# Kernel tuning notes

Hardware: AMD Instinct MI355X
Metric: run time of the kernel (lower is better)

Reference implementation:

```python
import jax, jax.numpy as jnp
import numpy as np

B, A, E = 16384, 8, 512


def setup_inputs() -> dict:
    key = jax.random.key(0)
    ks = jax.random.split(key, 6)
    return {
        "image_features": jax.random.normal(ks[0], (B, E), dtype=jnp.float32),
        "edge_attributes": jax.random.normal(ks[1], (B, A, E), dtype=jnp.float32),
        "linear_w": jax.random.normal(ks[2], (E, 2 * E), dtype=jnp.float32) * (1.0 / np.sqrt(2 * E)),
        "linear_b": jax.random.normal(ks[3], (E,), dtype=jnp.float32) * 0.01,
        "fwd_proj": jax.random.normal(ks[4], (A, E, E), dtype=jnp.float32) * (1.0 / np.sqrt(E)),
        "bwd_proj": jax.random.normal(ks[5], (A, E, E), dtype=jnp.float32) * (1.0 / np.sqrt(E)),
        "self_weighted": jnp.ones((1, A, 1), dtype=jnp.float32),
    }


def reference(image_features, edge_attributes, linear_w, linear_b, fwd_proj, bwd_proj, self_weighted):
    # Forward attribute GNN: broadcast src over attribute axis, concat, linear(2E->E)
    src = jnp.broadcast_to(image_features[:, None, :], edge_attributes.shape)  # [B,A,E]
    x = jnp.concatenate([src, edge_attributes], axis=-1)                       # [B,A,2E]
    agg = jnp.einsum('bak,ek->bae', x, linear_w) + linear_b                    # [B,A,E]
    attr_rep = jnp.einsum('bai,aij->baj', agg, fwd_proj)                       # [B,A,E]

    # Backward attribute GNN: per-type projection, ReLU, learned weighted sum over A
    proj = jnp.einsum('bai,aij->baj', attr_rep, bwd_proj)                      # [B,A,E]
    individuals = jnp.sum(jax.nn.relu(proj) * self_weighted, axis=1)           # [B,E]
    return attr_rep, individuals
```

## Files before the change

### kernel.cpp

```cpp
#include <hip/hip_runtime.h>
#include <cstdint>
#include <cstddef>

#define NB 16384
#define NA 8
#define NE 512
#define NK 1024
#define NN 4096

typedef __bf16 bf16x8 __attribute__((ext_vector_type(8)));
typedef float  f32x4  __attribute__((ext_vector_type(4)));
typedef uint16_t u16x8 __attribute__((ext_vector_type(8)));

__device__ __forceinline__ uint16_t cvt_bf16(float f) {
    uint32_t u = __builtin_bit_cast(uint32_t, f);
    u += 0x7fffu + ((u >> 16) & 1u);
    return (uint16_t)(u >> 16);
}

__device__ __forceinline__ int swz(int row) { return (row ^ (row >> 2)) & 3; }

__device__ __forceinline__ int cf_pos(int row, int c) {
    return ((row >> 1) << 3) + ((((row & 1) << 2) + c) ^ ((row >> 1) & 7));
}

__device__ __forceinline__ void gl_lds16(const void* g, void* l) {
    __builtin_amdgcn_global_load_lds(
        (__attribute__((address_space(1))) void*)(void*)g,
        (__attribute__((address_space(3))) void*)l, 16, 0, 0);
}

__global__ __launch_bounds__(256) void k_tcvt(const float* __restrict__ in,
                                              uint16_t* __restrict__ out,
                                              int R, int C) {
    __shared__ float tile[32][33];
    int mat = blockIdx.z;
    int c0 = blockIdx.x * 32, r0 = blockIdx.y * 32;
    int tx = threadIdx.x & 31, ty = threadIdx.x >> 5;
    const float* src = in + (size_t)mat * R * C;
    uint16_t* dst = out + (size_t)mat * R * C;
#pragma unroll
    for (int yy = 0; yy < 4; ++yy) {
        int r = ty + yy * 8;
        tile[r][tx] = src[(size_t)(r0 + r) * C + c0 + tx];
    }
    __syncthreads();
#pragma unroll
    for (int yy = 0; yy < 4; ++yy) {
        int c = ty + yy * 8;
        dst[(size_t)(c0 + c) * R + r0 + tx] = cvt_bf16(tile[tx][c]);
    }
}

__global__ __launch_bounds__(256) void k_cvt4(const float* __restrict__ in,
                                              uint16_t* __restrict__ out, int n4) {
    int i = blockIdx.x * 256 + threadIdx.x;
    if (i >= n4) return;
    float4 v = ((const float4*)in)[i];
    ushort4 o;
    o.x = cvt_bf16(v.x); o.y = cvt_bf16(v.y); o.z = cvt_bf16(v.z); o.w = cvt_bf16(v.w);
    ((ushort4*)out)[i] = o;
}

__global__ __launch_bounds__(256) void k_bvec(const float* __restrict__ lb,
                                              const float* __restrict__ fwd,
                                              float* __restrict__ bvec) {
    int a = blockIdx.x >> 4, i0 = (blockIdx.x & 15) * 32;
    int t = threadIdx.x;
    float s0 = 0.f, s1 = 0.f;
#pragma unroll 4
    for (int i = 0; i < 32; ++i) {
        float w = lb[i0 + i];
        const float* f = fwd + ((size_t)a * NE + i0 + i) * NE;
        s0 = fmaf(w, f[t], s0);
        s1 = fmaf(w, f[t + 256], s1);
    }
    atomicAdd(&bvec[a * NE + t], s0);
    atomicAdd(&bvec[a * NE + t + 256], s1);
}

__global__ __launch_bounds__(256) void k_prep(const uint16_t* __restrict__ lwT,
                                              const uint16_t* __restrict__ fwdT,
                                              uint16_t* __restrict__ TMT) {
    __shared__ alignas(16) uint16_t lA[128 * 32];
    __shared__ alignas(16) uint16_t lB[128 * 32];
    int bz = blockIdx.x;
    int nt = bz & 31, mt = bz >> 5;
    int m0 = mt * 128, n0 = nt * 128;
    int t = threadIdx.x, lane = t & 63;
    int w = t >> 6, wm = w >> 1, wn = w & 1;
    int lr = lane & 15, lc = lane >> 4;
    int sl = swz(lr);
    f32x4 acc[4][4] = {};
    for (int k0 = 0; k0 < NE; k0 += 32) {
        __syncthreads();
#pragma unroll
        for (int p = 0; p < 2; ++p) {
            int idx = p * 256 + t;
            int row = idx >> 2, c16 = (idx & 3) ^ swz(row);
            gl_lds16(lwT + (size_t)(m0 + row) * NE + k0 + c16 * 8, lA + idx * 8);
            gl_lds16(fwdT + (size_t)(n0 + row) * NE + k0 + c16 * 8, lB + idx * 8);
        }
        __syncthreads();
        bf16x8 af[4], bfr[4];
#pragma unroll
        for (int i = 0; i < 4; ++i)
            af[i] = *(const bf16x8*)&lA[(wm * 64 + i * 16 + lr) * 32 + ((lc ^ sl) << 3)];
#pragma unroll
        for (int j = 0; j < 4; ++j)
            bfr[j] = *(const bf16x8*)&lB[(wn * 64 + j * 16 + lr) * 32 + ((lc ^ sl) << 3)];
#pragma unroll
        for (int i = 0; i < 4; ++i)
#pragma unroll
            for (int j = 0; j < 4; ++j)
                acc[i][j] = __builtin_amdgcn_mfma_f32_16x16x32_bf16(af[i], bfr[j], acc[i][j], 0, 0, 0);
    }
#pragma unroll
    for (int i = 0; i < 4; ++i) {
        int mb = m0 + wm * 64 + i * 16 + lc * 4;
#pragma unroll
        for (int j = 0; j < 4; ++j) {
            int n = n0 + wn * 64 + j * 16 + lr;
            ushort4 v;
            v.x = cvt_bf16(acc[i][j][0]);
            v.y = cvt_bf16(acc[i][j][1]);
            v.z = cvt_bf16(acc[i][j][2]);
            v.w = cvt_bf16(acc[i][j][3]);
            *(ushort4*)&TMT[(size_t)n * NK + mb] = v;
        }
    }
}

template<bool WB>
__global__ __launch_bounds__(512) void k_mm4(const uint16_t* __restrict__ imgb,
                                             const float* __restrict__ edge,
                                             const uint16_t* __restrict__ TMT,
                                             const float* __restrict__ bvec,
                                             float* __restrict__ attr,
                                             uint16_t* __restrict__ attrb) {
    __shared__ alignas(16) uint16_t lA[2][128 * 32];
    __shared__ alignas(16) uint16_t lB[2][256 * 32];
    int o = blockIdx.x;
    int a = o & 7, idx = o >> 3;
    int jt = idx & 1, mt = idx >> 1;
    int m0 = mt * 128, jb = jt * 256;
    int t = threadIdx.x, lane = t & 63;
    int w = t >> 6, wm = w >> 2, wn = w & 3;
    int lr = lane & 15, lc = lane >> 4;
    int rpA = t >> 3, qA = (t & 7) ^ (rpA & 7);
    int srA = (rpA << 1) | (qA >> 2), scA = (qA & 3) << 3;
    int srB[2], scB[2];
#pragma unroll
    for (int p = 0; p < 2; ++p) {
        int u = t + p * 512;
        int rp = u >> 3, q = (u & 7) ^ (rp & 7);
        srB[p] = (rp << 1) | (q >> 2);
        scB[p] = (q & 3) << 3;
    }
    int er = t >> 2, ec = t & 3;
    int epos = cf_pos(er, ec) * 8;
    int aoff[4], boff[4];
#pragma unroll
    for (int i = 0; i < 4; ++i) {
        aoff[i] = cf_pos(wm * 64 + i * 16 + lr, lc) * 8;
        boff[i] = cf_pos(wn * 64 + i * 16 + lr, lc) * 8;
    }
    auto stage_img = [&](int buf, int s) {
        gl_lds16(imgb + (size_t)(m0 + srA) * NE + s * 32 + scA, &lA[buf][t * 8]);
    };
    auto stage_tmt = [&](int buf, int s) {
#pragma unroll
        for (int p = 0; p < 2; ++p)
            gl_lds16(TMT + (size_t)(a * NE + jb + srB[p]) * NK + s * 32 + scB[p],
                     &lB[buf][(t + p * 512) * 8]);
    };
    f32x4 acc[4][4] = {};
    stage_img(0, 0);
    stage_tmt(0, 0);
    for (int s = 0; s < 32; ++s) {
        int cur = s & 1, nb = cur ^ 1;
        __syncthreads();
        float4 e0, e1;
        bool eN = (s < 31) && (s + 1 >= 16);
        if (s < 31) {
            if (s + 1 < 16) {
                stage_img(nb, s + 1);
            } else {
                int kk = (s + 1 - 16) * 32;
                const float* sp = edge + ((size_t)(m0 + er) * NA + a) * NE + kk + ec * 8;
                e0 = ((const float4*)sp)[0];
                e1 = ((const float4*)sp)[1];
            }
            stage_tmt(nb, s + 1);
        }
        bf16x8 af[4], bfr[4];
#pragma unroll
        for (int i = 0; i < 4; ++i) af[i] = *(const bf16x8*)&lA[cur][aoff[i]];
#pragma unroll
        for (int j = 0; j < 4; ++j) bfr[j] = *(const bf16x8*)&lB[cur][boff[j]];
#pragma unroll
        for (int i = 0; i < 4; ++i)
#pragma unroll
            for (int j = 0; j < 4; ++j)
                acc[i][j] = __builtin_amdgcn_mfma_f32_16x16x32_bf16(af[i], bfr[j], acc[i][j], 0, 0, 0);
        if (eN) {
            u16x8 ov = {cvt_bf16(e0.x), cvt_bf16(e0.y), cvt_bf16(e0.z), cvt_bf16(e0.w),
                        cvt_bf16(e1.x), cvt_bf16(e1.y), cvt_bf16(e1.z), cvt_bf16(e1.w)};
            *(u16x8*)&lA[nb][epos] = ov;
        }
    }
#pragma unroll
    for (int j = 0; j < 4; ++j) {
        float bv = bvec[a * NE + jb + wn * 64 + j * 16 + lr];
#pragma unroll
        for (int i = 0; i < 4; ++i)
#pragma unroll
            for (int r = 0; r < 4; ++r)
                acc[i][j][r] += bv;
    }
#pragma unroll
    for (int i = 0; i < 4; ++i) {
#pragma unroll
        for (int r = 0; r < 4; ++r) {
            int bm = m0 + wm * 64 + i * 16 + lc * 4 + r;
            float* orow = attr + ((size_t)bm * NA + a) * NE + jb;
#pragma unroll
            for (int j = 0; j < 4; ++j)
                orow[wn * 64 + j * 16 + lr] = acc[i][j][r];
            if (WB) {
                uint16_t* brow = attrb + ((size_t)bm * NA + a) * NE + jb;
#pragma unroll
                for (int j = 0; j < 4; ++j)
                    brow[wn * 64 + j * 16 + lr] = cvt_bf16(acc[i][j][r]);
            }
        }
    }
}

template<bool AB>
__global__ __launch_bounds__(256) void k_ind4(const float* __restrict__ attrf,
                                              const uint16_t* __restrict__ attrb,
                                              const uint16_t* __restrict__ bwdT,
                                              const float* __restrict__ sw,
                                              float* __restrict__ ind) {
    __shared__ alignas(16) uint16_t lA[2][128 * 32];
    __shared__ alignas(16) uint16_t lB[2][128 * 32];
    int o = blockIdx.x;
    int xcd = o & 7, mt = o >> 3;
    int jt = xcd >> 1, ah = xcd & 1;
    int m0 = mt * 128, jb = jt * 128, a0 = ah * 4;
    int t = threadIdx.x, lane = t & 63;
    int w = t >> 6, wm = w >> 1, wn = w & 1;
    int lr = lane & 15, lc = lane >> 4;
    int srow[2], sc8[2];
#pragma unroll
    for (int p = 0; p < 2; ++p) {
        int u = p * 256 + t;
        int rp = u >> 3, q = (u & 7) ^ (rp & 7);
        srow[p] = (rp << 1) | (q >> 2);
        sc8[p] = (q & 3) << 3;
    }
    int erow[2], ec[2], epos[2];
#pragma unroll
    for (int p = 0; p < 2; ++p) {
        int u = p * 256 + t;
        erow[p] = u >> 2; ec[p] = u & 3;
        epos[p] = cf_pos(erow[p], ec[p]) * 8;
    }
    int aoff[4], boff[4];
#pragma unroll
    for (int i = 0; i < 4; ++i) {
        aoff[i] = cf_pos(wm * 64 + i * 16 + lr, lc) * 8;
        boff[i] = cf_pos(wn * 64 + i * 16 + lr, lc) * 8;
    }
    auto stage = [&](int buf, int s) {
        int aa = a0 + (s >> 4), kk = (s & 15) * 32;
        if (AB) {
#pragma unroll
            for (int p = 0; p < 2; ++p)
                gl_lds16(attrb + ((size_t)(m0 + srow[p]) * NA + aa) * NE + kk + sc8[p],
                         &lA[buf][(p * 256 + t) * 8]);
        } else {
#pragma unroll
            for (int p = 0; p < 2; ++p) {
                const float* sp = attrf + ((size_t)(m0 + erow[p]) * NA + aa) * NE + kk + ec[p] * 8;
                float4 v0 = ((const float4*)sp)[0];
                float4 v1 = ((const float4*)sp)[1];
                u16x8 ov = {cvt_bf16(v0.x), cvt_bf16(v0.y), cvt_bf16(v0.z), cvt_bf16(v0.w),
                            cvt_bf16(v1.x), cvt_bf16(v1.y), cvt_bf16(v1.z), cvt_bf16(v1.w)};
                *(u16x8*)&lA[buf][epos[p]] = ov;
            }
        }
#pragma unroll
        for (int p = 0; p < 2; ++p)
            gl_lds16(bwdT + (size_t)(aa * NE + jb + srow[p]) * NE + kk + sc8[p],
                     &lB[buf][(p * 256 + t) * 8]);
    };
    f32x4 res[4][4] = {};
    f32x4 acc[4][4] = {};
    stage(0, 0);
    for (int s = 0; s < 64; ++s) {
        int cur = s & 1;
        __syncthreads();
        if (s < 63) stage(cur ^ 1, s + 1);
        bf16x8 af[4], bfr[4];
#pragma unroll
        for (int i = 0; i < 4; ++i) af[i] = *(const bf16x8*)&lA[cur][aoff[i]];
#pragma unroll
        for (int j = 0; j < 4; ++j) bfr[j] = *(const bf16x8*)&lB[cur][boff[j]];
#pragma unroll
        for (int i = 0; i < 4; ++i)
#pragma unroll
            for (int j = 0; j < 4; ++j)
                acc[i][j] = __builtin_amdgcn_mfma_f32_16x16x32_bf16(af[i], bfr[j], acc[i][j], 0, 0, 0);
        if ((s & 15) == 15) {
            float wa = sw[a0 + (s >> 4)];
#pragma unroll
            for (int i = 0; i < 4; ++i)
#pragma unroll
                for (int j = 0; j < 4; ++j) {
#pragma unroll
                    for (int r = 0; r < 4; ++r)
                        res[i][j][r] += wa * fmaxf(acc[i][j][r], 0.f);
                    acc[i][j] = (f32x4){0.f, 0.f, 0.f, 0.f};
                }
        }
    }
#pragma unroll
    for (int i = 0; i < 4; ++i) {
#pragma unroll
        for (int r = 0; r < 4; ++r) {
            int bm = m0 + wm * 64 + i * 16 + lc * 4 + r;
            float* orow = ind + (size_t)bm * NE + jb;
#pragma unroll
            for (int j = 0; j < 4; ++j)
                atomicAdd(&orow[wn * 64 + j * 16 + lr], res[i][j][r]);
        }
    }
}

extern "C" void kernel_launch(void* const* d_in, const int* in_sizes, int n_in,
                              void* d_out, int out_size, void* d_ws, size_t ws_size,
                              hipStream_t stream) {
    (void)in_sizes; (void)n_in; (void)out_size;
    const float* img  = (const float*)d_in[0];
    const float* edge = (const float*)d_in[1];
    const float* lw   = (const float*)d_in[2];
    const float* lb   = (const float*)d_in[3];
    const float* fwd  = (const float*)d_in[4];
    const float* bwd  = (const float*)d_in[5];
    const float* sw   = (const float*)d_in[6];
    float* attr = (float*)d_out;
    float* ind  = attr + (size_t)NB * NA * NE;

    char* ws = (char*)d_ws;
    size_t off = 0;
    auto alloc = [&](size_t bytes) { void* p = ws + off; off += bytes; return p; };
    uint16_t* lwT  = (uint16_t*)alloc((size_t)NK * NE * 2);
    uint16_t* fwdT = (uint16_t*)alloc((size_t)NA * NE * NE * 2);
    uint16_t* bwdT = (uint16_t*)alloc((size_t)NA * NE * NE * 2);
    uint16_t* TMT  = (uint16_t*)alloc((size_t)NN * NK * 2);
    uint16_t* imgb = (uint16_t*)alloc((size_t)NB * NE * 2);
    float*    bvec = (float*)alloc((size_t)NN * 4);

    const size_t BIGB = (size_t)NB * NA * NE * 2;
    bool has_attrb = ws_size >= off + BIGB;
    uint16_t* attrb = has_attrb ? (uint16_t*)alloc(BIGB) : (uint16_t*)0;

    hipMemsetAsync(bvec, 0, (size_t)NN * 4, stream);
    hipMemsetAsync(ind, 0, (size_t)NB * NE * 4, stream);
    k_tcvt<<<dim3(NK / 32, NE / 32, 1), 256, 0, stream>>>(lw, lwT, NE, NK);
    k_tcvt<<<dim3(NE / 32, NE / 32, NA), 256, 0, stream>>>(fwd, fwdT, NE, NE);
    k_tcvt<<<dim3(NE / 32, NE / 32, NA), 256, 0, stream>>>(bwd, bwdT, NE, NE);
    k_cvt4<<<NB * NE / 4 / 256, 256, 0, stream>>>(img, imgb, NB * NE / 4);
    k_bvec<<<128, 256, 0, stream>>>(lb, fwd, bvec);
    k_prep<<<(NK / 128) * (NN / 128), 256, 0, stream>>>(lwT, fwdT, TMT);

    int mm_grid = 8 * 2 * (NB / 128);
    int ind_grid = (NB / 128) * (NE / 128) * 2;

    if (has_attrb) {
        k_mm4<true><<<mm_grid, 512, 0, stream>>>(imgb, edge, TMT, bvec, attr, attrb);
        k_ind4<true><<<ind_grid, 256, 0, stream>>>(attr, attrb, bwdT, sw, ind);
    } else {
        k_mm4<false><<<mm_grid, 512, 0, stream>>>(imgb, edge, TMT, bvec, attr, attrb);
        k_ind4<false><<<ind_grid, 256, 0, stream>>>(attr, attrb, bwdT, sw, ind);
    }
}
```

Measured before the change: 462.4 us.

## Use single-buffered K=64 stages with XOR swizzle in both GEMM kernels

```diff
diff --git a/kernel.cpp b/kernel.cpp
--- a/kernel.cpp
+++ b/kernel.cpp
@@ -19,10 +19,6 @@
 }
 
 __device__ __forceinline__ int swz(int row) { return (row ^ (row >> 2)) & 3; }
-
-__device__ __forceinline__ int cf_pos(int row, int c) {
-    return ((row >> 1) << 3) + ((((row & 1) << 2) + c) ^ ((row >> 1) & 7));
-}
 
 __device__ __forceinline__ void gl_lds16(const void* g, void* l) {
     __builtin_amdgcn_global_load_lds(
@@ -132,14 +128,14 @@
 }
 
 template<bool WB>
-__global__ __launch_bounds__(512) void k_mm4(const uint16_t* __restrict__ imgb,
+__global__ __launch_bounds__(512) void k_mm5(const uint16_t* __restrict__ imgb,
                                              const float* __restrict__ edge,
                                              const uint16_t* __restrict__ TMT,
                                              const float* __restrict__ bvec,
                                              float* __restrict__ attr,
                                              uint16_t* __restrict__ attrb) {
-    __shared__ alignas(16) uint16_t lA[2][128 * 32];
-    __shared__ alignas(16) uint16_t lB[2][256 * 32];
+    __shared__ alignas(16) uint16_t lA[128 * 64];
+    __shared__ alignas(16) uint16_t lB[256 * 64];
     int o = blockIdx.x;
     int a = o & 7, idx = o >> 3;
     int jt = idx & 1, mt = idx >> 1;
@@ -147,66 +143,81 @@
     int t = threadIdx.x, lane = t & 63;
     int w = t >> 6, wm = w >> 2, wn = w & 3;
     int lr = lane & 15, lc = lane >> 4;
-    int rpA = t >> 3, qA = (t & 7) ^ (rpA & 7);
-    int srA = (rpA << 1) | (qA >> 2), scA = (qA & 3) << 3;
-    int srB[2], scB[2];
+    int srA[2], scA[2];
 #pragma unroll
     for (int p = 0; p < 2; ++p) {
         int u = t + p * 512;
-        int rp = u >> 3, q = (u & 7) ^ (rp & 7);
-        srB[p] = (rp << 1) | (q >> 2);
-        scB[p] = (q & 3) << 3;
-    }
-    int er = t >> 2, ec = t & 3;
-    int epos = cf_pos(er, ec) * 8;
-    int aoff[4], boff[4];
+        srA[p] = u >> 3;
+        scA[p] = ((u & 7) ^ (srA[p] & 7)) << 3;
+    }
+    int srB[4], scB[4];
+#pragma unroll
+    for (int p = 0; p < 4; ++p) {
+        int u = t + p * 512;
+        srB[p] = u >> 3;
+        scB[p] = ((u & 7) ^ (srB[p] & 7)) << 3;
+    }
+    int erw[2], ecc[2], eps[2];
+#pragma unroll
+    for (int p = 0; p < 2; ++p) {
+        int u = t + p * 512;
+        erw[p] = u >> 3; ecc[p] = u & 7;
+        eps[p] = ((erw[p] << 3) + (ecc[p] ^ (erw[p] & 7))) << 3;
+    }
+    int arow[4], brow[4];
 #pragma unroll
     for (int i = 0; i < 4; ++i) {
-        aoff[i] = cf_pos(wm * 64 + i * 16 + lr, lc) * 8;
-        boff[i] = cf_pos(wn * 64 + i * 16 + lr, lc) * 8;
-    }
-    auto stage_img = [&](int buf, int s) {
-        gl_lds16(imgb + (size_t)(m0 + srA) * NE + s * 32 + scA, &lA[buf][t * 8]);
-    };
-    auto stage_tmt = [&](int buf, int s) {
-#pragma unroll
-        for (int p = 0; p < 2; ++p)
-            gl_lds16(TMT + (size_t)(a * NE + jb + srB[p]) * NK + s * 32 + scB[p],
-                     &lB[buf][(t + p * 512) * 8]);
+        arow[i] = wm * 64 + i * 16 + lr;
+        brow[i] = wn * 64 + i * 16 + lr;
+    }
+    float4 ereg[2][2];
+    auto load_edge = [&](int s) {
+        int kk = (s - 8) * 64;
+#pragma unroll
+        for (int p = 0; p < 2; ++p) {
+            const float* sp = edge + ((size_t)(m0 + erw[p]) * NA + a) * NE + kk + ecc[p] * 8;
+            ereg[p][0] = ((const float4*)sp)[0];
+            ereg[p][1] = ((const float4*)sp)[1];
+        }
     };
     f32x4 acc[4][4] = {};
-    stage_img(0, 0);
-    stage_tmt(0, 0);
-    for (int s = 0; s < 32; ++s) {
-        int cur = s & 1, nb = cur ^ 1;
-        __syncthreads();
-        float4 e0, e1;
-        bool eN = (s < 31) && (s + 1 >= 16);
-        if (s < 31) {
-            if (s + 1 < 16) {
-                stage_img(nb, s + 1);
-            } else {
-                int kk = (s + 1 - 16) * 32;
-                const float* sp = edge + ((size_t)(m0 + er) * NA + a) * NE + kk + ec * 8;
-                e0 = ((const float4*)sp)[0];
-                e1 = ((const float4*)sp)[1];
+    for (int s = 0; s < 16; ++s) {
+        __syncthreads();
+        if (s < 8) {
+#pragma unroll
+            for (int p = 0; p < 2; ++p)
+                gl_lds16(imgb + (size_t)(m0 + srA[p]) * NE + s * 64 + scA[p],
+                         &lA[(t + p * 512) * 8]);
+        } else {
+#pragma unroll
+            for (int p = 0; p < 2; ++p) {
+                u16x8 ov = {cvt_bf16(ereg[p][0].x), cvt_bf16(ereg[p][0].y),
+                            cvt_bf16(ereg[p][0].z), cvt_bf16(ereg[p][0].w),
+                            cvt_bf16(ereg[p][1].x), cvt_bf16(ereg[p][1].y),
+                            cvt_bf16(ereg[p][1].z), cvt_bf16(ereg[p][1].w)};
+                *(u16x8*)&lA[eps[p]] = ov;
             }
-            stage_tmt(nb, s + 1);
-        }
-        bf16x8 af[4], bfr[4];
-#pragma unroll
-        for (int i = 0; i < 4; ++i) af[i] = *(const bf16x8*)&lA[cur][aoff[i]];
-#pragma unroll
-        for (int j = 0; j < 4; ++j) bfr[j] = *(const bf16x8*)&lB[cur][boff[j]];
-#pragma unroll
-        for (int i = 0; i < 4; ++i)
+        }
+#pragma unroll
+        for (int p = 0; p < 4; ++p)
+            gl_lds16(TMT + (size_t)(a * NE + jb + srB[p]) * NK + s * 64 + scB[p],
+                     &lB[(t + p * 512) * 8]);
+        __syncthreads();
+        if (s >= 7 && s < 15) load_edge(s + 1);
+#pragma unroll
+        for (int h = 0; h < 2; ++h) {
+            bf16x8 af[4], bfr[4];
+#pragma unroll
+            for (int i = 0; i < 4; ++i)
+                af[i] = *(const bf16x8*)&lA[(arow[i] << 6) + ((((h << 2) + lc) ^ (arow[i] & 7)) << 3)];
 #pragma unroll
             for (int j = 0; j < 4; ++j)
-                acc[i][j] = __builtin_amdgcn_mfma_f32_16x16x32_bf16(af[i], bfr[j], acc[i][j], 0, 0, 0);
-        if (eN) {
-            u16x8 ov = {cvt_bf16(e0.x), cvt_bf16(e0.y), cvt_bf16(e0.z), cvt_bf16(e0.w),
-                        cvt_bf16(e1.x), cvt_bf16(e1.y), cvt_bf16(e1.z), cvt_bf16(e1.w)};
-            *(u16x8*)&lA[nb][epos] = ov;
+                bfr[j] = *(const bf16x8*)&lB[(brow[j] << 6) + ((((h << 2) + lc) ^ (brow[j] & 7)) << 3)];
+#pragma unroll
+            for (int i = 0; i < 4; ++i)
+#pragma unroll
+                for (int j = 0; j < 4; ++j)
+                    acc[i][j] = __builtin_amdgcn_mfma_f32_16x16x32_bf16(af[i], bfr[j], acc[i][j], 0, 0, 0);
         }
     }
 #pragma unroll
@@ -228,93 +239,101 @@
             for (int j = 0; j < 4; ++j)
                 orow[wn * 64 + j * 16 + lr] = acc[i][j][r];
             if (WB) {
-                uint16_t* brow = attrb + ((size_t)bm * NA + a) * NE + jb;
+                uint16_t* brw = attrb + ((size_t)bm * NA + a) * NE + jb;
 #pragma unroll
                 for (int j = 0; j < 4; ++j)
-                    brow[wn * 64 + j * 16 + lr] = cvt_bf16(acc[i][j][r]);
+                    brw[wn * 64 + j * 16 + lr] = cvt_bf16(acc[i][j][r]);
             }
         }
     }
 }
 
 template<bool AB>
-__global__ __launch_bounds__(256) void k_ind4(const float* __restrict__ attrf,
+__global__ __launch_bounds__(512) void k_ind5(const float* __restrict__ attrf,
                                               const uint16_t* __restrict__ attrb,
                                               const uint16_t* __restrict__ bwdT,
                                               const float* __restrict__ sw,
                                               float* __restrict__ ind) {
-    __shared__ alignas(16) uint16_t lA[2][128 * 32];
-    __shared__ alignas(16) uint16_t lB[2][128 * 32];
+    __shared__ alignas(16) uint16_t lA[128 * 64];
+    __shared__ alignas(16) uint16_t lB[256 * 64];
     int o = blockIdx.x;
-    int xcd = o & 7, mt = o >> 3;
-    int jt = xcd >> 1, ah = xcd & 1;
-    int m0 = mt * 128, jb = jt * 128, a0 = ah * 4;
+    int g = o & 7, mt = o >> 3;
+    int jt = g & 1, ah = g >> 1;
+    int m0 = mt * 128, jb = jt * 256, a0 = ah * 2;
     int t = threadIdx.x, lane = t & 63;
-    int w = t >> 6, wm = w >> 1, wn = w & 1;
+    int w = t >> 6, wm = w >> 2, wn = w & 3;
     int lr = lane & 15, lc = lane >> 4;
-    int srow[2], sc8[2];
+    int srA[2], scA[2];
 #pragma unroll
     for (int p = 0; p < 2; ++p) {
-        int u = p * 256 + t;
-        int rp = u >> 3, q = (u & 7) ^ (rp & 7);
-        srow[p] = (rp << 1) | (q >> 2);
-        sc8[p] = (q & 3) << 3;
-    }
-    int erow[2], ec[2], epos[2];
+        int u = t + p * 512;
+        srA[p] = u >> 3;
+        scA[p] = ((u & 7) ^ (srA[p] & 7)) << 3;
+    }
+    int srB[4], scB[4];
+#pragma unroll
+    for (int p = 0; p < 4; ++p) {
+        int u = t + p * 512;
+        srB[p] = u >> 3;
+        scB[p] = ((u & 7) ^ (srB[p] & 7)) << 3;
+    }
+    int erw[2], ecc[2], eps[2];
 #pragma unroll
     for (int p = 0; p < 2; ++p) {
-        int u = p * 256 + t;
-        erow[p] = u >> 2; ec[p] = u & 3;
-        epos[p] = cf_pos(erow[p], ec[p]) * 8;
-    }
-    int aoff[4], boff[4];
+        int u = t + p * 512;
+        erw[p] = u >> 3; ecc[p] = u & 7;
+        eps[p] = ((erw[p] << 3) + (ecc[p] ^ (erw[p] & 7))) << 3;
+    }
+    int arow[4], brow[4];
 #pragma unroll
     for (int i = 0; i < 4; ++i) {
-        aoff[i] = cf_pos(wm * 64 + i * 16 + lr, lc) * 8;
-        boff[i] = cf_pos(wn * 64 + i * 16 + lr, lc) * 8;
-    }
-    auto stage = [&](int buf, int s) {
-        int aa = a0 + (s >> 4), kk = (s & 15) * 32;
+        arow[i] = wm * 64 + i * 16 + lr;
+        brow[i] = wn * 64 + i * 16 + lr;
+    }
+    float wav[2] = {sw[a0], sw[a0 + 1]};
+    f32x4 res[4][4] = {};
+    f32x4 acc[4][4] = {};
+    for (int s = 0; s < 16; ++s) {
+        int aa = a0 + (s >> 3), kk = (s & 7) * 64;
+        __syncthreads();
         if (AB) {
 #pragma unroll
             for (int p = 0; p < 2; ++p)
-                gl_lds16(attrb + ((size_t)(m0 + srow[p]) * NA + aa) * NE + kk + sc8[p],
-                         &lA[buf][(p * 256 + t) * 8]);
+                gl_lds16(attrb + ((size_t)(m0 + srA[p]) * NA + aa) * NE + kk + scA[p],
+                         &lA[(t + p * 512) * 8]);
         } else {
 #pragma unroll
             for (int p = 0; p < 2; ++p) {
-                const float* sp = attrf + ((size_t)(m0 + erow[p]) * NA + aa) * NE + kk + ec[p] * 8;
+                const float* sp = attrf + ((size_t)(m0 + erw[p]) * NA + aa) * NE + kk + ecc[p] * 8;
                 float4 v0 = ((const float4*)sp)[0];
                 float4 v1 = ((const float4*)sp)[1];
                 u16x8 ov = {cvt_bf16(v0.x), cvt_bf16(v0.y), cvt_bf16(v0.z), cvt_bf16(v0.w),
                             cvt_bf16(v1.x), cvt_bf16(v1.y), cvt_bf16(v1.z), cvt_bf16(v1.w)};
-                *(u16x8*)&lA[buf][epos[p]] = ov;
+                *(u16x8*)&lA[eps[p]] = ov;
             }
         }
 #pragma unroll
-        for (int p = 0; p < 2; ++p)
-            gl_lds16(bwdT + (size_t)(aa * NE + jb + srow[p]) * NE + kk + sc8[p],
-                     &lB[buf][(p * 256 + t) * 8]);
-    };
-    f32x4 res[4][4] = {};
-    f32x4 acc[4][4] = {};
-    stage(0, 0);
-    for (int s = 0; s < 64; ++s) {
-        int cur = s & 1;
-        __syncthreads();
-        if (s < 63) stage(cur ^ 1, s + 1);
-        bf16x8 af[4], bfr[4];
-#pragma unroll
-        for (int i = 0; i < 4; ++i) af[i] = *(const bf16x8*)&lA[cur][aoff[i]];
-#pragma unroll
-        for (int j = 0; j < 4; ++j) bfr[j] = *(const bf16x8*)&lB[cur][boff[j]];
-#pragma unroll
-        for (int i = 0; i < 4; ++i)
+        for (int p = 0; p < 4; ++p)
+            gl_lds16(bwdT + (size_t)(aa * NE + jb + srB[p]) * NE + kk + scB[p],
+                     &lB[(t + p * 512) * 8]);
+        __syncthreads();
+#pragma unroll
+        for (int h = 0; h < 2; ++h) {
+            bf16x8 af[4], bfr[4];
+#pragma unroll
+            for (int i = 0; i < 4; ++i)
+                af[i] = *(const bf16x8*)&lA[(arow[i] << 6) + ((((h << 2) + lc) ^ (arow[i] & 7)) << 3)];
 #pragma unroll
             for (int j = 0; j < 4; ++j)
-                acc[i][j] = __builtin_amdgcn_mfma_f32_16x16x32_bf16(af[i], bfr[j], acc[i][j], 0, 0, 0);
-        if ((s & 15) == 15) {
-            float wa = sw[a0 + (s >> 4)];
+                bfr[j] = *(const bf16x8*)&lB[(brow[j] << 6) + ((((h << 2) + lc) ^ (brow[j] & 7)) << 3)];
+#pragma unroll
+            for (int i = 0; i < 4; ++i)
+#pragma unroll
+                for (int j = 0; j < 4; ++j)
+                    acc[i][j] = __builtin_amdgcn_mfma_f32_16x16x32_bf16(af[i], bfr[j], acc[i][j], 0, 0, 0);
+        }
+        if ((s & 7) == 7) {
+            float wa = wav[s >> 3];
 #pragma unroll
             for (int i = 0; i < 4; ++i)
 #pragma unroll
@@ -377,13 +396,13 @@
     k_prep<<<(NK / 128) * (NN / 128), 256, 0, stream>>>(lwT, fwdT, TMT);
 
     int mm_grid = 8 * 2 * (NB / 128);
-    int ind_grid = (NB / 128) * (NE / 128) * 2;
+    int ind_grid = 8 * (NB / 128);
 
     if (has_attrb) {
-        k_mm4<true><<<mm_grid, 512, 0, stream>>>(imgb, edge, TMT, bvec, attr, attrb);
-        k_ind4<true><<<ind_grid, 256, 0, stream>>>(attr, attrb, bwdT, sw, ind);
+        k_mm5<true><<<mm_grid, 512, 0, stream>>>(imgb, edge, TMT, bvec, attr, attrb);
+        k_ind5<true><<<ind_grid, 512, 0, stream>>>(attr, attrb, bwdT, sw, ind);
     } else {
-        k_mm4<false><<<mm_grid, 512, 0, stream>>>(imgb, edge, TMT, bvec, attr, attrb);
-        k_ind4<false><<<ind_grid, 256, 0, stream>>>(attr, attrb, bwdT, sw, ind);
-    }
-}
+        k_mm5<false><<<mm_grid, 512, 0, stream>>>(imgb, edge, TMT, bvec, attr, attrb);
+        k_ind5<false><<<ind_grid, 512, 0, stream>>>(attr, attrb, bwdT, sw, ind);
+    }
+}
```

Result: slower. 509.3 us (+10.1%).
